# Performance work log

Hardware: AMD Instinct MI355X
Metric: run time of the kernel (lower is better)

The kernel has to match this reference:

```python
import jax, jax.numpy as jnp
import numpy as np

F = 20            # number of fields
V_FIELD = 5000    # vocab per field
TOTAL = F * V_FIELD
D = 64            # embedding dim (emd)
B = 8192          # batch
OFFSETS = jnp.arange(F, dtype=jnp.int32) * V_FIELD  # field offsets into shared table
_iu, _ju = np.triu_indices(F, k=1)                  # P = F*(F-1)/2 = 190 pairs
I_IDX = jnp.asarray(_iu, dtype=jnp.int32)
J_IDX = jnp.asarray(_ju, dtype=jnp.int32)


def setup_inputs() -> dict:
    key = jax.random.key(0)
    k1, k2, k3 = jax.random.split(key, 3)
    x = jax.random.randint(k1, (B, F), 0, V_FIELD, dtype=jnp.int32)
    # F field-aware embedding tables, each over the full offset vocab
    W = jax.random.normal(k2, (F, TOTAL, D), dtype=jnp.float32) * 0.01
    # linear term table (emd=1)
    Wl = jax.random.normal(k3, (TOTAL, 1), dtype=jnp.float32) * 0.01
    bias = jnp.zeros((1,), dtype=jnp.float32)
    return {"x": x, "W": W, "Wl": Wl, "bias": bias}


def reference(x, W, Wl, bias):
    idx = x + OFFSETS[None, :]                      # [B, F] global ids
    # embedding[:, j*F+i] == table j looked up at field-i's id
    a = W[J_IDX[None, :], idx[:, I_IDX]]            # [B, P, D] = V_j[x_i]
    b = W[I_IDX[None, :], idx[:, J_IDX]]            # [B, P, D] = V_i[x_j]
    interaction = jnp.sum(a * b, axis=(1, 2))[:, None]  # [B, 1]
    lin = Wl[idx].sum(axis=1)                       # [B, 1]
    return jax.nn.sigmoid(lin + bias + interaction)
```

## Files before the change

kernel.cpp:

```cpp
#include <hip/hip_runtime.h>
#include <math.h>


#define FF 20
#define V_FIELD 5000
#define TOTAL (FF * V_FIELD)
#define DD 64
#define SPB 4
#define NP 190
#define NPP 192

__global__ __launch_bounds__(256, 4) void ffm_kernel(
    const int* __restrict__ x,
    const float* __restrict__ W,
    const float* __restrict__ Wl,
    const float* __restrict__ bias,
    float* __restrict__ out)
{
    __shared__ int g[SPB][FF];
    __shared__ short pi[NPP], pj[NPP];
    __shared__ unsigned offA[SPB][NPP], offB[SPB][NPP];

    const int t = threadIdx.x;
    const int sbase = blockIdx.x * SPB;

    if (t < SPB * FF) {
        const int s = t / FF, f = t % FF;
        g[s][f] = x[(sbase + s) * FF + f] + f * V_FIELD;
    }
    if (t < NPP) {
        int pp = (t >= NP) ? 0 : t;
        int i = 0;
        while (pp >= FF - 1 - i) { pp -= FF - 1 - i; ++i; }
        pi[t] = (short)i;
        pj[t] = (short)(i + 1 + pp);
    }
    __syncthreads();

    const int wave = t >> 6;
    const int lane = t & 63;
    const int b = sbase + wave;

    for (int q = lane; q < 2 * NPP; q += 64) {
        if (q < NPP) {
            const int p = q;
            offA[wave][p] = (unsigned)(pj[p] * TOTAL + g[wave][pi[p]]) * (DD * 4);
        } else {
            const int p = q - NPP;
            offB[wave][p] = (unsigned)(pi[p] * TOTAL + g[wave][pj[p]]) * (DD * 4);
        }
    }
    __syncthreads();

    const int grp = lane >> 4;
    const unsigned chunk = (lane & 15) * 16;
    const char* Wb = (const char*)W;

    float a0 = 0.f, a1 = 0.f, a2 = 0.f, a3 = 0.f;

#pragma unroll 4
    for (int it = 0; it < 47; ++it) {
        const int p = it * 4 + grp;
        const float4 va = *(const float4*)(Wb + (offA[wave][p] + chunk));
        const float4 vb = *(const float4*)(Wb + (offB[wave][p] + chunk));
        a0 = fmaf(va.x, vb.x, a0);
        a1 = fmaf(va.y, vb.y, a1);
        a2 = fmaf(va.z, vb.z, a2);
        a3 = fmaf(va.w, vb.w, a3);
    }
    if (grp < 2) {
        const int p = 188 + grp;
        const float4 va = *(const float4*)(Wb + (offA[wave][p] + chunk));
        const float4 vb = *(const float4*)(Wb + (offB[wave][p] + chunk));
        a0 = fmaf(va.x, vb.x, a0);
        a1 = fmaf(va.y, vb.y, a1);
        a2 = fmaf(va.z, vb.z, a2);
        a3 = fmaf(va.w, vb.w, a3);
    }
    float acc = (a0 + a1) + (a2 + a3);

    if (lane < FF) acc += Wl[g[wave][lane]];

#pragma unroll
    for (int off = 32; off > 0; off >>= 1)
        acc += __shfl_down(acc, off, 64);

    if (lane == 0)
        out[b] = 1.f / (1.f + expf(-(acc + bias[0])));
}

extern "C" void kernel_launch(void* const* d_in, const int* in_sizes, int n_in,
                              void* d_out, int out_size, void* d_ws, size_t ws_size,
                              hipStream_t stream) {
    const int*   x    = (const int*)d_in[0];
    const float* W    = (const float*)d_in[1];
    const float* Wl   = (const float*)d_in[2];
    const float* bias = (const float*)d_in[3];
    float* out = (float*)d_out;

    const int nB = out_size;
    dim3 grid(nB / SPB), block(256);
    hipLaunchKernelGGL(ffm_kernel, grid, block, 0, stream,
                       x, W, Wl, bias, out);
}
```

Measured before the change: 658.8 us.

## Split FFM pairs across XCDs with streaming slice prefetch and atomic reduction

Work is repartitioned so that each block handles one eighth of the field pairs, selected by blockIdx & 7 on the assumption that blocks are dealt round-robin to the XCDs, for 32 samples. Partial dot products are accumulated into a workspace with atomics, and a second kernel adds the linear term and applies the sigmoid. Inside the pair loop, each block also streams coalesced reads across the whole embedding slice for the current pair. This is meant to pull the slice into that XCD's L2 so the random 256-byte row gathers hit cache. The cost is a much larger volume of extra reads plus a memset, atomics and two more launches, and the benefit depends on the block-to-XCD mapping and on timing across blocks.

```diff
diff --git a/kernel.cpp b/kernel.cpp
--- a/kernel.cpp
+++ b/kernel.cpp
@@ -6,87 +6,125 @@
 #define V_FIELD 5000
 #define TOTAL (FF * V_FIELD)
 #define DD 64
-#define SPB 4
+#define ROW_B 256
 #define NP 190
-#define NPP 192
+#define NXCD 8
+#define SPB 32
+#define MAXPP 24
+#define SLICE_F4 80000
 
-__global__ __launch_bounds__(256, 4) void ffm_kernel(
+__global__ __launch_bounds__(256, 4) void ffm_pairs(
     const int* __restrict__ x,
     const float* __restrict__ W,
-    const float* __restrict__ Wl,
-    const float* __restrict__ bias,
-    float* __restrict__ out)
+    float* __restrict__ ws)
 {
     __shared__ int g[SPB][FF];
-    __shared__ short pi[NPP], pj[NPP];
-    __shared__ unsigned offA[SPB][NPP], offB[SPB][NPP];
+    __shared__ int pii[MAXPP], pjj[MAXPP];
+    __shared__ unsigned bA[MAXPP], bB[MAXPP], wA[MAXPP], wB[MAXPP];
+    __shared__ unsigned offA[SPB][MAXPP], offB[SPB][MAXPP];
 
-    const int t = threadIdx.x;
-    const int sbase = blockIdx.x * SPB;
+    const int t   = threadIdx.x;
+    const int n   = blockIdx.x;
+    const int xcd = n & 7;
+    const int c   = n >> 3;
+    const int s0g = c * SPB;
+    const int npx = (NP - xcd + NXCD - 1) / NXCD;
 
-    if (t < SPB * FF) {
-        const int s = t / FF, f = t % FF;
-        g[s][f] = x[(sbase + s) * FF + f] + f * V_FIELD;
+    for (int u = t; u < SPB * FF; u += 256) {
+        const int s = u / FF, f = u - s * FF;
+        g[s][f] = x[(s0g + s) * FF + f] + f * V_FIELD;
     }
-    if (t < NPP) {
-        int pp = (t >= NP) ? 0 : t;
-        int i = 0;
+    if (t < npx) {
+        int p = xcd + t * NXCD;
+        int pp = p, i = 0;
         while (pp >= FF - 1 - i) { pp -= FF - 1 - i; ++i; }
-        pi[t] = (short)i;
-        pj[t] = (short)(i + 1 + pp);
+        const int j = i + 1 + pp;
+        pii[t] = i; pjj[t] = j;
+        const unsigned a  = (unsigned)(j * TOTAL) * ROW_B;
+        const unsigned b2 = (unsigned)(i * TOTAL) * ROW_B;
+        bA[t] = a;  bB[t] = b2;
+        wA[t] = a  + (unsigned)(i * V_FIELD) * ROW_B;
+        wB[t] = b2 + (unsigned)(j * V_FIELD) * ROW_B;
     }
     __syncthreads();
 
-    const int wave = t >> 6;
-    const int lane = t & 63;
-    const int b = sbase + wave;
-
-    for (int q = lane; q < 2 * NPP; q += 64) {
-        if (q < NPP) {
-            const int p = q;
-            offA[wave][p] = (unsigned)(pj[p] * TOTAL + g[wave][pi[p]]) * (DD * 4);
-        } else {
-            const int p = q - NPP;
-            offB[wave][p] = (unsigned)(pi[p] * TOTAL + g[wave][pj[p]]) * (DD * 4);
-        }
+    for (int u = t; u < SPB * npx; u += 256) {
+        const int s = u / npx, q = u - s * npx;
+        offA[s][q] = bA[q] + ((unsigned)g[s][pii[q]] << 8);
+        offB[s][q] = bB[q] + ((unsigned)g[s][pjj[q]] << 8);
     }
     __syncthreads();
 
-    const int grp = lane >> 4;
+    const int lane = t & 63;
+    const int wave = t >> 6;
+    const int grp  = lane >> 4;
     const unsigned chunk = (lane & 15) * 16;
+    const int sA = wave * 8 + grp;
+    const int sB = sA + 4;
     const char* Wb = (const char*)W;
+    const unsigned wl = ((unsigned)c << 8) | (unsigned)t;
 
-    float a0 = 0.f, a1 = 0.f, a2 = 0.f, a3 = 0.f;
+    float a00=0.f, a01=0.f, a02=0.f, a03=0.f;
+    float a10=0.f, a11=0.f, a12=0.f, a13=0.f;
+    float wk = 0.f;
 
-#pragma unroll 4
-    for (int it = 0; it < 47; ++it) {
-        const int p = it * 4 + grp;
-        const float4 va = *(const float4*)(Wb + (offA[wave][p] + chunk));
-        const float4 vb = *(const float4*)(Wb + (offB[wave][p] + chunk));
-        a0 = fmaf(va.x, vb.x, a0);
-        a1 = fmaf(va.y, vb.y, a1);
-        a2 = fmaf(va.z, vb.z, a2);
-        a3 = fmaf(va.w, vb.w, a3);
+    for (int q = 0; q < npx; ++q) {
+        {
+            const float4* fA = (const float4*)(Wb + wA[q]);
+            const float4* fB = (const float4*)(Wb + wB[q]);
+            const float4 u0 = fA[wl];
+            const float4 u1 = fB[wl];
+            wk += (u0.x + u0.y) + (u0.z + u0.w)
+                + (u1.x + u1.y) + (u1.z + u1.w);
+            if (wl < (unsigned)(SLICE_F4 - 65536)) {
+                const float4 u2 = fA[wl + 65536u];
+                const float4 u3 = fB[wl + 65536u];
+                wk += (u2.x + u2.y) + (u2.z + u2.w)
+                    + (u3.x + u3.y) + (u3.z + u3.w);
+            }
+        }
+        const float4 va0 = *(const float4*)(Wb + (offA[sA][q] + chunk));
+        const float4 vb0 = *(const float4*)(Wb + (offB[sA][q] + chunk));
+        const float4 va1 = *(const float4*)(Wb + (offA[sB][q] + chunk));
+        const float4 vb1 = *(const float4*)(Wb + (offB[sB][q] + chunk));
+        a00 = fmaf(va0.x, vb0.x, a00);
+        a01 = fmaf(va0.y, vb0.y, a01);
+        a02 = fmaf(va0.z, vb0.z, a02);
+        a03 = fmaf(va0.w, vb0.w, a03);
+        a10 = fmaf(va1.x, vb1.x, a10);
+        a11 = fmaf(va1.y, vb1.y, a11);
+        a12 = fmaf(va1.z, vb1.z, a12);
+        a13 = fmaf(va1.w, vb1.w, a13);
     }
-    if (grp < 2) {
-        const int p = 188 + grp;
-        const float4 va = *(const float4*)(Wb + (offA[wave][p] + chunk));
-        const float4 vb = *(const float4*)(Wb + (offB[wave][p] + chunk));
-        a0 = fmaf(va.x, vb.x, a0);
-        a1 = fmaf(va.y, vb.y, a1);
-        a2 = fmaf(va.z, vb.z, a2);
-        a3 = fmaf(va.w, vb.w, a3);
+
+    asm volatile("" :: "v"(wk));
+
+    float r0 = (a00 + a01) + (a02 + a03);
+    float r1 = (a10 + a11) + (a12 + a13);
+#pragma unroll
+    for (int off = 8; off > 0; off >>= 1) {
+        r0 += __shfl_xor(r0, off, 64);
+        r1 += __shfl_xor(r1, off, 64);
     }
-    float acc = (a0 + a1) + (a2 + a3);
+    if ((lane & 15) == 0) {
+        atomicAdd(&ws[s0g + sA], r0);
+        atomicAdd(&ws[s0g + sB], r1);
+    }
+}
 
-    if (lane < FF) acc += Wl[g[wave][lane]];
-
+__global__ __launch_bounds__(256) void ffm_final(
+    const int* __restrict__ x,
+    const float* __restrict__ Wl,
+    const float* __restrict__ bias,
+    const float* __restrict__ ws,
+    float* __restrict__ out)
+{
+    const int b = blockIdx.x * 256 + threadIdx.x;
+    float acc = ws[b] + bias[0];
 #pragma unroll
-    for (int off = 32; off > 0; off >>= 1)
-        acc += __shfl_down(acc, off, 64);
-
-    if (lane == 0)
-        out[b] = 1.f / (1.f + expf(-(acc + bias[0])));
+    for (int f = 0; f < FF; ++f)
+        acc += Wl[x[b * FF + f] + f * V_FIELD];
+    out[b] = 1.f / (1.f + expf(-acc));
 }
 
 extern "C" void kernel_launch(void* const* d_in, const int* in_sizes, int n_in,
@@ -99,7 +137,13 @@
     float* out = (float*)d_out;
 
     const int nB = out_size;
-    dim3 grid(nB / SPB), block(256);
-    hipLaunchKernelGGL(ffm_kernel, grid, block, 0, stream,
-                       x, W, Wl, bias, out);
+    float* wsf = (float*)d_ws;
+
+    hipMemsetAsync(wsf, 0, nB * sizeof(float), stream);
+
+    const int nchunk = nB / SPB;
+    hipLaunchKernelGGL(ffm_pairs, dim3(nchunk * NXCD), dim3(256), 0, stream,
+                       x, W, wsf);
+    hipLaunchKernelGGL(ffm_final, dim3(nB / 256), dim3(256), 0, stream,
+                       x, Wl, bias, wsf, out);
 }
```

Measured after the change: 714.3 us. +8.4%, slower.
